# Optimization experiments

Hardware: AMD Instinct MI355X
Metric: run time of the kernel (lower is better)

The kernel has to match this reference:

```python
import jax, jax.numpy as jnp
import numpy as np
from jax import lax

HEADS = 4
NEG_SLOPE = 0.2


def _layernorm(x, g, b, eps=1e-5):
    m = x.mean(-1, keepdims=True)
    v = ((x - m) ** 2).mean(-1, keepdims=True)
    return (x - m) * lax.rsqrt(v + eps) * g + b


def setup_inputs() -> dict:
    key = jax.random.key(0)
    ks = jax.random.split(key, 10)
    B, N, T, H, E, ED, K = 1, 1000, 32, 128, 16000, 16, 3
    s_h = 1.0 / np.sqrt(H)
    s_e = 1.0 / np.sqrt(ED)
    return {
        "x": jax.random.normal(ks[0], (B, N, T, H), jnp.float32),
        "edge_index": jax.random.randint(ks[1], (2, E), 0, N, dtype=jnp.int32),
        "edge_attr": jax.random.normal(ks[2], (E, ED), jnp.float32),
        "conv_w": jax.random.normal(ks[3], (H, H, K), jnp.float32) * (1.0 / np.sqrt(H * K)),
        "conv_b": jnp.zeros((H,), jnp.float32),
        "ln1_g": jnp.ones((H,), jnp.float32),
        "ln1_b": jnp.zeros((H,), jnp.float32),
        "Wl": jax.random.normal(ks[4], (H, H), jnp.float32) * s_h,
        "Wr": jax.random.normal(ks[5], (H, H), jnp.float32) * s_h,
        "We": jax.random.normal(ks[6], (ED, H), jnp.float32) * s_e,
        "att": jax.random.normal(ks[7], (HEADS, H // HEADS), jnp.float32) * s_h,
        "gat_b": jnp.zeros((H,), jnp.float32),
        "ln2_g": jnp.ones((H,), jnp.float32),
        "ln2_b": jnp.zeros((H,), jnp.float32),
    }


def reference(x, edge_index, edge_attr, conv_w, conv_b, ln1_g, ln1_b,
              Wl, Wr, We, att, gat_b, ln2_g, ln2_b):
    B, N, T, H = x.shape
    K = HEADS
    D = H // K
    E = edge_attr.shape[0]

    # ---- temporal sub-block: per-node Conv1d over time ('same' padding) ----
    xt = x.reshape(B * N, T, H).transpose(0, 2, 1)            # [BN, H, T]
    y = lax.conv_general_dilated(xt, conv_w, (1,), 'SAME',
                                 dimension_numbers=('NCH', 'OIH', 'NCH'))
    y = y + conv_b[None, :, None]
    y = y.transpose(0, 2, 1).reshape(B, N, T, H)
    x = _layernorm(x + y, ln1_g, ln1_b)

    # ---- spatial sub-block: GATv2 at every timestep (mega-batch of G graphs) ----
    G = B * T
    xs = x.transpose(0, 2, 1, 3).reshape(G, N, H)             # [G, N, H]

    # add self-loops, fill_value='mean' (mean of incoming edge attrs per node)
    dst0 = edge_index[1]
    cnt = jax.ops.segment_sum(jnp.ones((E,), edge_attr.dtype), dst0, num_segments=N)
    loop_attr = jax.ops.segment_sum(edge_attr, dst0, num_segments=N) / jnp.maximum(cnt, 1.0)[:, None]
    ea = jnp.concatenate([edge_attr, loop_attr], axis=0)       # [E+N, ED]
    loops = jnp.arange(N, dtype=edge_index.dtype)
    src = jnp.concatenate([edge_index[0], loops])
    dst = jnp.concatenate([edge_index[1], loops])

    gl = jnp.einsum('gnh,hkd->gnkd', xs, Wl.reshape(H, K, D))  # source transform
    gr = jnp.einsum('gnh,hkd->gnkd', xs, Wr.reshape(H, K, D))  # target transform
    ee = jnp.einsum('ef,fkd->ekd', ea, We.reshape(-1, K, D))   # edge transform

    e_src = jnp.swapaxes(gl[:, src], 0, 1)                     # [E', G, K, D]
    e_dst = jnp.swapaxes(gr[:, dst], 0, 1)                     # [E', G, K, D]
    s = jax.nn.leaky_relu(e_src + e_dst + ee[:, None], NEG_SLOPE)
    logits = jnp.einsum('egkd,kd->egk', s, att)                # [E', G, K]

    # scatter-softmax over incoming edges per target node (self-loops => non-empty)
    mx = jax.ops.segment_max(logits, dst, num_segments=N)[dst]
    ex = jnp.exp(logits - mx)
    den = jax.ops.segment_sum(ex, dst, num_segments=N)[dst]
    alpha = ex / den

    aggr = jax.ops.segment_sum(e_src * alpha[..., None], dst, num_segments=N)  # [N, G, K, D]
    out = jnp.swapaxes(aggr, 0, 1).reshape(G, N, H) + gat_b

    out = out.reshape(B, T, N, H).transpose(0, 2, 1, 3)        # back to (B, N, T, H)
    return _layernorm(x + out, ln2_g, ln2_b)
```

## Files before the change

kernel.cpp:

```cpp
#include <hip/hip_runtime.h>
#include <math.h>

#define N_NODES 1000
#define T_STEPS 32
#define H_DIM   128
#define E_EDGES 16000
#define ED_DIM  16
#define G_GRAPHS 32
#define EP_EDGES (E_EDGES + N_NODES)
#define NEG_SLOPE 0.2f
#define LN_EPS 1e-5f
#define CSR_CAP 128

typedef __attribute__((ext_vector_type(8))) short bf16x8;
typedef __attribute__((ext_vector_type(16))) float f32x16;
typedef __attribute__((ext_vector_type(4))) float f32x4;
typedef __attribute__((ext_vector_type(4))) unsigned u32x4;
typedef unsigned short u16;

__device__ inline short f2bf(float f) {
    unsigned u = __float_as_uint(f);
    u = (u + 0x7FFFu + ((u >> 16) & 1u)) >> 16;
    return (short)u;
}
__device__ inline float bf2f(u16 u) { return __uint_as_float(((unsigned)u) << 16); }
__device__ inline float bflo(unsigned u) { return __uint_as_float(u << 16); }
__device__ inline float bfhi(unsigned u) { return __uint_as_float(u & 0xFFFF0000u); }

__global__ __launch_bounds__(1024) void k_prep(
    const float* __restrict__ conv_w, const float* __restrict__ Wl,
    const float* __restrict__ Wr, const int* __restrict__ dst,
    short* __restrict__ wc, short* __restrict__ wg,
    int* __restrict__ cnt, int* __restrict__ csr) {
    int b = blockIdx.x;
    if (b < 80) {
        int i = b * 1024 + threadIdx.x;
        if (i < 4 * 24 * 64 * 8) {
            int r = i & 7, lane = (i >> 3) & 63;
            int t = i >> 9;
            int kstep = t % 24, ct = t / 24;
            int k = kstep >> 3, hs = kstep & 7;
            int hi = hs * 16 + ((lane >> 5) << 3) + r;
            int o = ct * 32 + (lane & 31);
            wc[i] = f2bf(conv_w[(o * H_DIM + hi) * 3 + k]);
        } else {
            int j = i - 4 * 24 * 64 * 8;
            int r = j & 7, lane = (j >> 3) & 63;
            int ks = (j >> 9) & 7, ct = j >> 12;
            int hi = ks * 16 + ((lane >> 5) << 3) + r;
            int o = ct * 32 + (lane & 31);
            wg[j] = f2bf(o < H_DIM ? Wl[hi * H_DIM + o] : Wr[hi * H_DIM + o - H_DIM]);
        }
        return;
    }
    int e = (b - 80) * 1024 + threadIdx.x;
    if (e < E_EDGES) {
        int d = dst[e];
        int slot = atomicAdd(&cnt[d], 1);
        if (slot < CSR_CAP) csr[d * CSR_CAP + slot] = e;
    }
}

__global__ __launch_bounds__(256) void k_fuse(
    const float* __restrict__ x, const short* __restrict__ wc, const short* __restrict__ wg,
    const float* __restrict__ conv_b, const float* __restrict__ ln1_g,
    const float* __restrict__ ln1_b, const float* __restrict__ edge_attr,
    const float* __restrict__ We, int* __restrict__ csr, const int* __restrict__ cnt,
    u16* __restrict__ x1b, u16* __restrict__ gl, u16* __restrict__ gr,
    u16* __restrict__ ee) {
    __shared__ __align__(16) short xb[34 * 136];
    __shared__ __align__(16) float yb[32 * 136];
    __shared__ int buf[CSR_CAP];
    __shared__ float laf[16];
    int b = blockIdx.x;
    int tid = threadIdx.x;

    if (b >= 2000) {
        int e = (b - 2000) * 2 + (tid >> 7);
        int h = tid & 127;
        if (e >= E_EDGES) return;
        const float* ea = &edge_attr[e * ED_DIM];
        float acc = 0.f;
#pragma unroll
        for (int f = 0; f < ED_DIM; ++f) acc += ea[f] * We[f * H_DIM + h];
        __builtin_nontemporal_store((u16)f2bf(acc), &ee[(size_t)e * H_DIM + h]);
        return;
    }
    if (b >= 1000) {
        int n = b - 1000;
        int off = n * CSR_CAP, deg = cnt[n];
        bool fast = (deg <= 64);
        if (fast) {
            if (tid < 64) {
                int v = (tid < deg) ? csr[off + tid] : 0x7FFFFFFF;
                int rank = 0;
#pragma unroll
                for (int j = 0; j < 64; ++j) {
                    int vj = __shfl(v, j);
                    rank += (vj < v) ? 1 : 0;
                }
                if (tid < deg) buf[rank] = v;
            }
        } else {
            for (int i = tid; i < deg && i < CSR_CAP; i += 256) buf[i] = csr[off + i];
        }
        __syncthreads();
        if (!fast && tid == 0) {
            int dd = deg < CSR_CAP ? deg : CSR_CAP;
            for (int i = 1; i < dd; ++i) {
                int key = buf[i], j = i - 1;
                while (j >= 0 && buf[j] > key) { buf[j + 1] = buf[j]; --j; }
                buf[j + 1] = key;
            }
        }
        __syncthreads();
        if (tid < deg && tid < CSR_CAP) csr[off + tid] = buf[tid];
        if (tid < 64) {
            int q = tid >> 4, f = tid & 15;
            float a = 0.f;
            for (int i = q; i < deg; i += 4) a += edge_attr[buf[i] * ED_DIM + f];
            a += __shfl_xor(a, 16);
            a += __shfl_xor(a, 32);
            if (tid < 16) laf[tid] = a / fmaxf((float)deg, 1.0f);
        }
        __syncthreads();
        if (tid < H_DIM) {
            float acc = 0.f;
#pragma unroll
            for (int f = 0; f < ED_DIM; ++f) acc += laf[f] * We[f * H_DIM + tid];
            ee[(size_t)(E_EDGES + n) * H_DIM + tid] = (u16)f2bf(acc);
        }
        return;
    }

    int n = b;
    int w = tid >> 6, lane = tid & 63;
    int arow = lane & 31;
    int aks = (lane >> 5) << 3;

    {
        const f32x4* xs4 = (const f32x4*)(x + (size_t)n * T_STEPS * H_DIM);
        for (int i4 = tid; i4 < T_STEPS * H_DIM / 4; i4 += 256) {
            f32x4 v = __builtin_nontemporal_load(&xs4[i4]);
            int t = i4 >> 5, h = (i4 * 4) & 127;
            uint2 pp;
            pp.x = (unsigned)(unsigned short)f2bf(v.x) | ((unsigned)(unsigned short)f2bf(v.y) << 16);
            pp.y = (unsigned)(unsigned short)f2bf(v.z) | ((unsigned)(unsigned short)f2bf(v.w) << 16);
            *(uint2*)&xb[(t + 1) * 136 + h] = pp;
        }
        if (tid < 68) {
            ((unsigned*)xb)[tid] = 0u;
            ((unsigned*)(xb + 33 * 136))[tid] = 0u;
        }
    }
    __syncthreads();

    f32x16 acc = {};
    for (int kk = 0; kk < 3; ++kk) {
#pragma unroll
        for (int hs = 0; hs < 8; ++hs) {
            int kstep = kk * 8 + hs;
            bf16x8 a = *(const bf16x8*)&xb[(arow + kk) * 136 + hs * 16 + aks];
            bf16x8 bb = *(const bf16x8*)&wc[((w * 24 + kstep) * 64 + lane) * 8];
            acc = __builtin_amdgcn_mfma_f32_32x32x16_bf16(a, bb, acc, 0, 0, 0);
        }
    }
    {
        int oc = w * 32 + (lane & 31);
        float cb = conv_b[oc];
#pragma unroll
        for (int r = 0; r < 16; ++r) {
            int t = (r & 3) + 8 * (r >> 2) + 4 * (lane >> 5);
            yb[t * 136 + oc] = acc[r] + cb;
        }
    }
    __syncthreads();

    float rr0[8], rr1[8];
#pragma unroll
    for (int idx = 0; idx < 8; ++idx) {
        int t = w + idx * 4;
        rr0[idx] = bf2f((u16)xb[(t + 1) * 136 + lane]) + yb[t * 136 + lane];
        rr1[idx] = bf2f((u16)xb[(t + 1) * 136 + lane + 64]) + yb[t * 136 + lane + 64];
    }
    __syncthreads();
    float g0c = ln1_g[lane], g1c = ln1_g[lane + 64];
    float b0c = ln1_b[lane], b1c = ln1_b[lane + 64];
#pragma unroll
    for (int idx = 0; idx < 8; ++idx) {
        int t = w + idx * 4;
        float r0 = rr0[idx], r1 = rr1[idx];
        float s = r0 + r1, s2 = r0 * r0 + r1 * r1;
#pragma unroll
        for (int mm = 1; mm < 64; mm <<= 1) {
            s += __shfl_xor(s, mm);
            s2 += __shfl_xor(s2, mm);
        }
        float mean = s * (1.f / 128.f);
        float var = s2 * (1.f / 128.f) - mean * mean;
        float rs = rsqrtf(var + LN_EPS);
        float o0 = (r0 - mean) * rs * g0c + b0c;
        float o1 = (r1 - mean) * rs * g1c + b1c;
        xb[t * 136 + lane] = f2bf(o0);
        xb[t * 136 + lane + 64] = f2bf(o1);
    }
    __syncthreads();

    for (int c = tid; c < 512; c += 256) {
        int t = c >> 4, p = c & 15;
        u32x4 v = *(const u32x4*)&xb[t * 136 + p * 8];
        *(u32x4*)&x1b[((size_t)n * T_STEPS + t) * H_DIM + p * 8] = v;
    }

    f32x16 cl = {}, cr = {};
#pragma unroll
    for (int ks = 0; ks < 8; ++ks) {
        bf16x8 a = *(const bf16x8*)&xb[arow * 136 + ks * 16 + aks];
        bf16x8 b0 = *(const bf16x8*)&wg[(((2 * w) * 8 + ks) * 64 + lane) * 8];
        bf16x8 b1 = *(const bf16x8*)&wg[(((2 * w + 1) * 8 + ks) * 64 + lane) * 8];
        cl = __builtin_amdgcn_mfma_f32_32x32x16_bf16(a, b0, cl, 0, 0, 0);
        cr = __builtin_amdgcn_mfma_f32_32x32x16_bf16(a, b1, cr, 0, 0, 0);
    }
    __syncthreads();
    {
        u16* st = (u16*)yb;
        int m = w >> 1;
        int c0 = (w & 1) * 64 + (lane & 31);
#pragma unroll
        for (int r = 0; r < 16; ++r) {
            int t = (r & 3) + 8 * (r >> 2) + 4 * (lane >> 5);
            st[(m * 32 + t) * 136 + c0] = (u16)f2bf(cl[r]);
            st[(m * 32 + t) * 136 + c0 + 32] = (u16)f2bf(cr[r]);
        }
    }
    __syncthreads();
    {
        const u16* st = (const u16*)yb;
        for (int c = tid; c < 1024; c += 256) {
            int m = c >> 9, t = (c >> 4) & 31, p = c & 15;
            u32x4 v = *(const u32x4*)&st[(m * 32 + t) * 136 + p * 8];
            u16* d = m ? gr : gl;
            *(u32x4*)&d[((size_t)t * N_NODES + n) * H_DIM + p * 8] = v;
        }
    }
}

__global__ __launch_bounds__(128) void k_gat(
    const u16* __restrict__ gl, const u16* __restrict__ gr, const u16* __restrict__ ee,
    const int* __restrict__ src_arr, const int* __restrict__ csr,
    const int* __restrict__ cnt, const float* __restrict__ att,
    const float* __restrict__ gat_b, const u16* __restrict__ x1b,
    const float* __restrict__ ln2_g, const float* __restrict__ ln2_b,
    float* __restrict__ out) {
    int bid = blockIdx.x;
    int q = bid & 3;
    int n = bid >> 2;
    int tid = threadIdx.x;
    int gs = tid >> 4;
    int r = tid & 15;
    int h0 = ((r >> 2) << 5) + ((r & 3) << 3);
    int g = q + 4 * gs;

    __shared__ int es[64], ss[64];
    int off = n * CSR_CAP, deg = cnt[n];
    int tot = deg + 1;

    float av[8], grv[8];
    {
        float4 a0 = *(const float4*)&att[h0];
        float4 a1 = *(const float4*)&att[h0 + 4];
        av[0] = a0.x; av[1] = a0.y; av[2] = a0.z; av[3] = a0.w;
        av[4] = a1.x; av[5] = a1.y; av[6] = a1.z; av[7] = a1.w;
        u32x4 g4 = *(const u32x4*)&gr[((size_t)g * N_NODES + n) * H_DIM + h0];
        grv[0] = bflo(g4.x); grv[1] = bfhi(g4.x); grv[2] = bflo(g4.y); grv[3] = bfhi(g4.y);
        grv[4] = bflo(g4.z); grv[5] = bfhi(g4.z); grv[6] = bflo(g4.w); grv[7] = bfhi(g4.w);
    }
    const u16* glg = gl + (size_t)g * N_NODES * H_DIM + h0;
    const u16* eeh = ee + h0;

    size_t ob = ((size_t)n * T_STEPS + g) * H_DIM + h0;
    u32x4 xv = __builtin_nontemporal_load((const u32x4*)&x1b[ob]);

    float m = -INFINITY, l = 0.f;
    float ac[8] = {0.f, 0.f, 0.f, 0.f, 0.f, 0.f, 0.f, 0.f};

    auto LDQ = [&](u32x4& G, u32x4& E, int idx) {
        int s_ = ss[idx], e_ = es[idx];
        G = *(const u32x4*)&glg[(size_t)s_ * H_DIM];
        E = __builtin_nontemporal_load((const u32x4*)&eeh[(size_t)e_ * H_DIM]);
    };
    auto PROC = [&](u32x4 gc, u32x4 ec) {
        float gvv[8];
        gvv[0] = bflo(gc.x); gvv[1] = bfhi(gc.x); gvv[2] = bflo(gc.y); gvv[3] = bfhi(gc.y);
        gvv[4] = bflo(gc.z); gvv[5] = bfhi(gc.z); gvv[6] = bflo(gc.w); gvv[7] = bfhi(gc.w);
        float evv[8];
        evv[0] = bflo(ec.x); evv[1] = bfhi(ec.x); evv[2] = bflo(ec.y); evv[3] = bfhi(ec.y);
        evv[4] = bflo(ec.z); evv[5] = bfhi(ec.z); evv[6] = bflo(ec.w); evv[7] = bfhi(ec.w);
        float p = 0.f;
#pragma unroll
        for (int j = 0; j < 8; ++j) {
            float sf = gvv[j] + grv[j] + evv[j];
            sf = fmaxf(sf, NEG_SLOPE * sf);
            p = fmaf(sf, av[j], p);
        }
        p += __shfl_xor(p, 1);
        p += __shfl_xor(p, 2);
        float mn = fmaxf(m, p);
        float sc = __expf(m - mn);
        float wq = __expf(p - mn);
        l = l * sc + wq;
#pragma unroll
        for (int j = 0; j < 8; ++j) ac[j] = ac[j] * sc + wq * gvv[j];
        m = mn;
    };

    for (int base = 0; base < tot; base += 64) {
        int c = min(64, tot - base);
        __syncthreads();
        if (tid < c) {
            int i = base + tid;
            int e = (i < deg) ? csr[off + i] : (E_EDGES + n);
            es[tid] = e;
            ss[tid] = (i < deg) ? src_arr[e] : n;
        }
        __syncthreads();
        int c1 = c - 1;
        u32x4 gA, eA, gB, eB, gC, eC, gD, eD;
        LDQ(gA, eA, 0);
        LDQ(gB, eB, min(1, c1));
        LDQ(gC, eC, min(2, c1));
        LDQ(gD, eD, min(3, c1));
        for (int i = 0; i < c; i += 4) {
            u32x4 g0 = gA, e0 = eA, g1 = gB, e1 = eB;
            u32x4 g2 = gC, e2 = eC, g3 = gD, e3 = eD;
            LDQ(gA, eA, min(i + 4, c1));
            LDQ(gB, eB, min(i + 5, c1));
            LDQ(gC, eC, min(i + 6, c1));
            LDQ(gD, eD, min(i + 7, c1));
            PROC(g0, e0);
            if (i + 1 < c) PROC(g1, e1);
            if (i + 2 < c) PROC(g2, e2);
            if (i + 3 < c) PROC(g3, e3);
        }
    }

    float linv = 1.0f / l;
    float4 gb0 = *(const float4*)&gat_b[h0];
    float4 gb1 = *(const float4*)&gat_b[h0 + 4];
    float xr[8];
    xr[0] = bflo(xv.x); xr[1] = bfhi(xv.x); xr[2] = bflo(xv.y); xr[3] = bfhi(xv.y);
    xr[4] = bflo(xv.z); xr[5] = bfhi(xv.z); xr[6] = bflo(xv.w); xr[7] = bfhi(xv.w);
    float gbv[8] = {gb0.x, gb0.y, gb0.z, gb0.w, gb1.x, gb1.y, gb1.z, gb1.w};
    float rv[8];
    float s1 = 0.f, s2v = 0.f;
#pragma unroll
    for (int j = 0; j < 8; ++j) {
        rv[j] = xr[j] + ac[j] * linv + gbv[j];
        s1 += rv[j];
        s2v += rv[j] * rv[j];
    }
#pragma unroll
    for (int mm = 1; mm < 16; mm <<= 1) {
        s1 += __shfl_xor(s1, mm);
        s2v += __shfl_xor(s2v, mm);
    }
    float mean = s1 * (1.f / 128.f);
    float var = s2v * (1.f / 128.f) - mean * mean;
    float rs = rsqrtf(var + LN_EPS);
    float4 g20 = *(const float4*)&ln2_g[h0];
    float4 g21 = *(const float4*)&ln2_g[h0 + 4];
    float4 b20 = *(const float4*)&ln2_b[h0];
    float4 b21 = *(const float4*)&ln2_b[h0 + 4];
    f32x4 o0, o1;
    o0.x = (rv[0] - mean) * rs * g20.x + b20.x;
    o0.y = (rv[1] - mean) * rs * g20.y + b20.y;
    o0.z = (rv[2] - mean) * rs * g20.z + b20.z;
    o0.w = (rv[3] - mean) * rs * g20.w + b20.w;
    o1.x = (rv[4] - mean) * rs * g21.x + b21.x;
    o1.y = (rv[5] - mean) * rs * g21.y + b21.y;
    o1.z = (rv[6] - mean) * rs * g21.z + b21.z;
    o1.w = (rv[7] - mean) * rs * g21.w + b21.w;
    __builtin_nontemporal_store(o0, (f32x4*)&out[ob]);
    __builtin_nontemporal_store(o1, (f32x4*)&out[ob + 4]);
}

extern "C" void kernel_launch(void* const* d_in, const int* in_sizes, int n_in,
                              void* d_out, int out_size, void* d_ws, size_t ws_size,
                              hipStream_t stream) {
    const float* x         = (const float*)d_in[0];
    const int*   ei        = (const int*)d_in[1];
    const float* edge_attr = (const float*)d_in[2];
    const float* conv_w    = (const float*)d_in[3];
    const float* conv_b    = (const float*)d_in[4];
    const float* ln1_g     = (const float*)d_in[5];
    const float* ln1_b     = (const float*)d_in[6];
    const float* Wl        = (const float*)d_in[7];
    const float* Wr        = (const float*)d_in[8];
    const float* We        = (const float*)d_in[9];
    const float* att       = (const float*)d_in[10];
    const float* gat_b     = (const float*)d_in[11];
    const float* ln2_g     = (const float*)d_in[12];
    const float* ln2_b     = (const float*)d_in[13];
    float* out = (float*)d_out;

    const int* src = ei;
    const int* dst = ei + E_EDGES;

    u16* x1b    = (u16*)d_ws;
    u16* glb    = x1b + 4096000;
    u16* grb    = glb + 4096000;
    u16* eeb    = grb + 4096000;
    int* cnt    = (int*)(eeb + 2176000);
    int* csr    = cnt + 1000;
    short* wc   = (short*)(csr + 128000);
    short* wg   = wc + 49152;

    hipMemsetAsync(cnt, 0, N_NODES * sizeof(int), stream);
    k_prep<<<96, 1024, 0, stream>>>(conv_w, Wl, Wr, dst, wc, wg, cnt, csr);
    k_fuse<<<10000, 256, 0, stream>>>(x, wc, wg, conv_b, ln1_g, ln1_b, edge_attr, We,
                                      csr, cnt, x1b, glb, grb, eeb);
    k_gat<<<4 * N_NODES, 128, 0, stream>>>(glb, grb, eeb, src, csr, cnt,
                                           att, gat_b, x1b, ln2_g, ln2_b, out);
}
```

Baseline: 77.80 us.

## Build CSR per node inside fuse kernel, drop memset and cut edge-transform blocks

Removes the hipMemsetAsync and the global atomic CSR build from the prep kernel. Each per-node block in the fuse kernel now scans the whole dst array with shared-memory atomics to collect its incoming edges and writes both the degree and the sorted list. The edge-transform blocks now process 16 edges per block instead of 2, shrinking the fuse grid from 10000 to 3000 blocks. This saves one launch, the memset and global atomic contention, at the cost of every node block reading all 16000 dst entries (64KB each, mostly from L2).

```diff
diff --git a/kernel.cpp b/kernel.cpp
--- a/kernel.cpp
+++ b/kernel.cpp
@@ -29,35 +29,23 @@
 
 __global__ __launch_bounds__(1024) void k_prep(
     const float* __restrict__ conv_w, const float* __restrict__ Wl,
-    const float* __restrict__ Wr, const int* __restrict__ dst,
-    short* __restrict__ wc, short* __restrict__ wg,
-    int* __restrict__ cnt, int* __restrict__ csr) {
-    int b = blockIdx.x;
-    if (b < 80) {
-        int i = b * 1024 + threadIdx.x;
-        if (i < 4 * 24 * 64 * 8) {
-            int r = i & 7, lane = (i >> 3) & 63;
-            int t = i >> 9;
-            int kstep = t % 24, ct = t / 24;
-            int k = kstep >> 3, hs = kstep & 7;
-            int hi = hs * 16 + ((lane >> 5) << 3) + r;
-            int o = ct * 32 + (lane & 31);
-            wc[i] = f2bf(conv_w[(o * H_DIM + hi) * 3 + k]);
-        } else {
-            int j = i - 4 * 24 * 64 * 8;
-            int r = j & 7, lane = (j >> 3) & 63;
-            int ks = (j >> 9) & 7, ct = j >> 12;
-            int hi = ks * 16 + ((lane >> 5) << 3) + r;
-            int o = ct * 32 + (lane & 31);
-            wg[j] = f2bf(o < H_DIM ? Wl[hi * H_DIM + o] : Wr[hi * H_DIM + o - H_DIM]);
-        }
-        return;
-    }
-    int e = (b - 80) * 1024 + threadIdx.x;
-    if (e < E_EDGES) {
-        int d = dst[e];
-        int slot = atomicAdd(&cnt[d], 1);
-        if (slot < CSR_CAP) csr[d * CSR_CAP + slot] = e;
+    const float* __restrict__ Wr, short* __restrict__ wc, short* __restrict__ wg) {
+    int i = blockIdx.x * 1024 + threadIdx.x;
+    if (i < 4 * 24 * 64 * 8) {
+        int r = i & 7, lane = (i >> 3) & 63;
+        int t = i >> 9;
+        int kstep = t % 24, ct = t / 24;
+        int k = kstep >> 3, hs = kstep & 7;
+        int hi = hs * 16 + ((lane >> 5) << 3) + r;
+        int o = ct * 32 + (lane & 31);
+        wc[i] = f2bf(conv_w[(o * H_DIM + hi) * 3 + k]);
+    } else {
+        int j = i - 4 * 24 * 64 * 8;
+        int r = j & 7, lane = (j >> 3) & 63;
+        int ks = (j >> 9) & 7, ct = j >> 12;
+        int hi = ks * 16 + ((lane >> 5) << 3) + r;
+        int o = ct * 32 + (lane & 31);
+        wg[j] = f2bf(o < H_DIM ? Wl[hi * H_DIM + o] : Wr[hi * H_DIM + o - H_DIM]);
     }
 }
 
@@ -65,34 +53,52 @@
     const float* __restrict__ x, const short* __restrict__ wc, const short* __restrict__ wg,
     const float* __restrict__ conv_b, const float* __restrict__ ln1_g,
     const float* __restrict__ ln1_b, const float* __restrict__ edge_attr,
-    const float* __restrict__ We, int* __restrict__ csr, const int* __restrict__ cnt,
+    const float* __restrict__ We, const int* __restrict__ dst,
+    int* __restrict__ csr, int* __restrict__ cnt,
     u16* __restrict__ x1b, u16* __restrict__ gl, u16* __restrict__ gr,
     u16* __restrict__ ee) {
     __shared__ __align__(16) short xb[34 * 136];
     __shared__ __align__(16) float yb[32 * 136];
     __shared__ int buf[CSR_CAP];
     __shared__ float laf[16];
+    __shared__ int scnt;
     int b = blockIdx.x;
     int tid = threadIdx.x;
 
     if (b >= 2000) {
-        int e = (b - 2000) * 2 + (tid >> 7);
+        int e0 = (b - 2000) * 16 + (tid >> 7);
         int h = tid & 127;
-        if (e >= E_EDGES) return;
-        const float* ea = &edge_attr[e * ED_DIM];
-        float acc = 0.f;
-#pragma unroll
-        for (int f = 0; f < ED_DIM; ++f) acc += ea[f] * We[f * H_DIM + h];
-        __builtin_nontemporal_store((u16)f2bf(acc), &ee[(size_t)e * H_DIM + h]);
+#pragma unroll
+        for (int k = 0; k < 16; k += 2) {
+            int e = e0 + k;
+            const float* ea = &edge_attr[e * ED_DIM];
+            float acc = 0.f;
+#pragma unroll
+            for (int f = 0; f < ED_DIM; ++f) acc += ea[f] * We[f * H_DIM + h];
+            __builtin_nontemporal_store((u16)f2bf(acc), &ee[(size_t)e * H_DIM + h]);
+        }
         return;
     }
     if (b >= 1000) {
         int n = b - 1000;
-        int off = n * CSR_CAP, deg = cnt[n];
+        if (tid == 0) scnt = 0;
+        __syncthreads();
+        const uint4* d4 = (const uint4*)dst;
+        for (int i = tid; i < E_EDGES / 4; i += 256) {
+            uint4 v = d4[i];
+            int e0 = i * 4;
+            if ((int)v.x == n) { int s = atomicAdd(&scnt, 1); if (s < CSR_CAP) buf[s] = e0; }
+            if ((int)v.y == n) { int s = atomicAdd(&scnt, 1); if (s < CSR_CAP) buf[s] = e0 + 1; }
+            if ((int)v.z == n) { int s = atomicAdd(&scnt, 1); if (s < CSR_CAP) buf[s] = e0 + 2; }
+            if ((int)v.w == n) { int s = atomicAdd(&scnt, 1); if (s < CSR_CAP) buf[s] = e0 + 3; }
+        }
+        __syncthreads();
+        int deg = min(scnt, CSR_CAP);
+        if (tid == 0) cnt[n] = deg;
         bool fast = (deg <= 64);
         if (fast) {
             if (tid < 64) {
-                int v = (tid < deg) ? csr[off + tid] : 0x7FFFFFFF;
+                int v = (tid < deg) ? buf[tid] : 0x7FFFFFFF;
                 int rank = 0;
 #pragma unroll
                 for (int j = 0; j < 64; ++j) {
@@ -102,19 +108,16 @@
                 if (tid < deg) buf[rank] = v;
             }
         } else {
-            for (int i = tid; i < deg && i < CSR_CAP; i += 256) buf[i] = csr[off + i];
-        }
-        __syncthreads();
-        if (!fast && tid == 0) {
-            int dd = deg < CSR_CAP ? deg : CSR_CAP;
-            for (int i = 1; i < dd; ++i) {
-                int key = buf[i], j = i - 1;
-                while (j >= 0 && buf[j] > key) { buf[j + 1] = buf[j]; --j; }
-                buf[j + 1] = key;
+            if (tid == 0) {
+                for (int i = 1; i < deg; ++i) {
+                    int key = buf[i], j = i - 1;
+                    while (j >= 0 && buf[j] > key) { buf[j + 1] = buf[j]; --j; }
+                    buf[j + 1] = key;
+                }
             }
         }
         __syncthreads();
-        if (tid < deg && tid < CSR_CAP) csr[off + tid] = buf[tid];
+        if (tid < deg) csr[n * CSR_CAP + tid] = buf[tid];
         if (tid < 64) {
             int q = tid >> 4, f = tid & 15;
             float a = 0.f;
@@ -415,10 +418,9 @@
     short* wc   = (short*)(csr + 128000);
     short* wg   = wc + 49152;
 
-    hipMemsetAsync(cnt, 0, N_NODES * sizeof(int), stream);
-    k_prep<<<96, 1024, 0, stream>>>(conv_w, Wl, Wr, dst, wc, wg, cnt, csr);
-    k_fuse<<<10000, 256, 0, stream>>>(x, wc, wg, conv_b, ln1_g, ln1_b, edge_attr, We,
-                                      csr, cnt, x1b, glb, grb, eeb);
+    k_prep<<<80, 1024, 0, stream>>>(conv_w, Wl, Wr, wc, wg);
+    k_fuse<<<3000, 256, 0, stream>>>(x, wc, wg, conv_b, ln1_g, ln1_b, edge_attr, We,
+                                     dst, csr, cnt, x1b, glb, grb, eeb);
     k_gat<<<4 * N_NODES, 128, 0, stream>>>(glb, grb, eeb, src, csr, cnt,
                                            att, gat_b, x1b, ln2_g, ln2_b, out);
 }
```

Result: faster. 72.98 us (-6.2%).
